# Kernel optimization log

Measured on AMD Instinct MI355X. Metric: run time of the kernel, lower is better.

## Reference

```python
import jax, jax.numpy as jnp
import numpy as np

NBITS = 16  # posit word size passed to posit_forward
ES = 1      # posit exponent-field size (standard posit16 uses es=1)


def posit_quant(x, nbits=NBITS, es=ES):
    """Round-trip float -> posit(nbits, es) -> float, vectorized.

    Emulates posit quantization: regime length determines how many fraction
    bits remain, mantissa is rounded to that precision, magnitude clamped to
    [minpos, maxpos]. Straight-through estimator keeps gradients useful.
    """
    absx = jnp.abs(x)
    sign = jnp.sign(x)
    safe = jnp.maximum(absx, 1e-30)
    scale = jnp.floor(jnp.log2(safe))                 # binary exponent
    useed_log2 = float(2 ** es)
    regime = jnp.floor(scale / useed_log2)
    rlen = jnp.where(regime >= 0, regime + 2.0, 1.0 - regime)  # regime bits
    fbits = jnp.clip(nbits - 1 - es - rlen, 0.0, 28.0)          # fraction bits left
    pw = jnp.exp2(fbits)
    m = safe * jnp.exp2(-scale)                       # mantissa in [1, 2)
    mq = 1.0 + jnp.round((m - 1.0) * pw) / pw
    maxscale = float((nbits - 2) * (2 ** es))         # maxpos = 2^((n-2)*2^es)
    mag = jnp.clip(mq * jnp.exp2(scale), jnp.exp2(-maxscale), jnp.exp2(maxscale))
    q = jnp.where(absx == 0.0, 0.0, sign * mag)
    return x + jax.lax.stop_gradient(q - x)           # straight-through


def posit_linear(x, W, b):
    # posit_forward: quantize operands, GEMM, quantize the accumulated output
    xq = posit_quant(x)
    Wq = posit_quant(W)
    bq = posit_quant(b)
    return posit_quant(xq @ Wq.T + bq)


def setup_inputs() -> dict:
    key = jax.random.key(0)
    ks = jax.random.split(key, 7)

    def w(k, o, i):
        return jax.random.normal(k, (o, i), jnp.float32) * (1.0 / np.sqrt(i))

    return {
        "x": jax.random.normal(ks[0], (4096, 2048), jnp.float32),
        "W0": w(ks[1], 8192, 2048),
        "b0": jax.random.normal(ks[2], (8192,), jnp.float32) * 0.01,
        "W1": w(ks[3], 8192, 8192),
        "b1": jax.random.normal(ks[4], (8192,), jnp.float32) * 0.01,
        "W2": w(ks[5], 2048, 8192),
        "b2": jax.random.normal(ks[6], (2048,), jnp.float32) * 0.01,
    }


def reference(x, W0, b0, W1, b1, W2, b2):
    # layer 0: posit linear + relu (clamp(min=0))
    h = jax.nn.relu(posit_linear(x, W0, b0))
    # layer 1: posit linear + relu
    h = jax.nn.relu(posit_linear(h, W1, b1))
    # layer 2: posit linear, identity activation
    return posit_linear(h, W2, b2)
```

## Files before the change

### kernel.cpp

```cpp
#include <hip/hip_runtime.h>
#include <hip/hip_bf16.h>
#include <cstdint>
#include <cstddef>

using bf16 = __hip_bfloat16;
typedef __attribute__((ext_vector_type(8))) short short8;
typedef __attribute__((ext_vector_type(4))) float f32x4;

__device__ __forceinline__ float posit_quant_f32(float x) {
  float absx = fabsf(x);
  float safe = fmaxf(absx, 1e-30f);
  uint32_t bits = __float_as_uint(safe);
  int scale = (int)((bits >> 23) & 0xFFu) - 127;
  int regime = scale >> 1;
  int rlen = (regime >= 0) ? (regime + 2) : (1 - regime);
  int fbits = 14 - rlen;
  fbits = fbits < 0 ? 0 : fbits;
  float pw = (float)(1 << fbits);
  float m = __uint_as_float((bits & 0x007FFFFFu) | 0x3F800000u);
  float mq = rintf((m - 1.0f) * pw) * (1.0f / pw) + 1.0f;
  float mag = mq * __uint_as_float((uint32_t)(scale + 127) << 23);
  mag = fminf(fmaxf(mag, 0x1p-28f), 0x1p28f);
  return (absx == 0.0f) ? 0.0f : copysignf(mag, x);
}

__device__ __forceinline__ ushort4 pq_bf16x4(float4 v) {
  ushort4 o;
  o.x = __builtin_bit_cast(unsigned short, __float2bfloat16(posit_quant_f32(v.x)));
  o.y = __builtin_bit_cast(unsigned short, __float2bfloat16(posit_quant_f32(v.y)));
  o.z = __builtin_bit_cast(unsigned short, __float2bfloat16(posit_quant_f32(v.z)));
  o.w = __builtin_bit_cast(unsigned short, __float2bfloat16(posit_quant_f32(v.w)));
  return o;
}

__global__ void kquant_all(const float* __restrict__ s0, bf16* __restrict__ d0,
                           const float* __restrict__ s1, bf16* __restrict__ d1,
                           const float* __restrict__ s2, bf16* __restrict__ d2,
                           const float* __restrict__ s3, bf16* __restrict__ d3,
                           long c0, long c1, long c2, long c3) {
  long i = (long)blockIdx.x * blockDim.x + threadIdx.x;
  long stride = (long)gridDim.x * blockDim.x;
  for (; i < c3; i += stride) {
    const float* s; bf16* d; long j;
    if (i < c0)      { s = s0; d = d0; j = i; }
    else if (i < c1) { s = s1; d = d1; j = i - c0; }
    else if (i < c2) { s = s2; d = d2; j = i - c1; }
    else             { s = s3; d = d3; j = i - c2; }
    float4 v = ((const float4*)s)[j];
    ((ushort4*)d)[j] = pq_bf16x4(v);
  }
}

__global__ void kcombine(const float* __restrict__ p, const float* __restrict__ bias,
                         float* __restrict__ out, long n4, long halfn, int cmask) {
  long i = (long)blockIdx.x * blockDim.x + threadIdx.x;
  long stride = (long)gridDim.x * blockDim.x;
  for (; i < n4; i += stride) {
    float4 a = ((const float4*)p)[i];
    float4 b = ((const float4*)(p + halfn))[i];
    int c0 = (int)(i & cmask) * 4;
    float4 o;
    o.x = posit_quant_f32(a.x + b.x + posit_quant_f32(bias[c0 + 0]));
    o.y = posit_quant_f32(a.y + b.y + posit_quant_f32(bias[c0 + 1]));
    o.z = posit_quant_f32(a.z + b.z + posit_quant_f32(bias[c0 + 2]));
    o.w = posit_quant_f32(a.w + b.w + posit_quant_f32(bias[c0 + 3]));
    ((float4*)out)[i] = o;
  }
}

typedef __attribute__((address_space(1))) uint32_t gu32;
typedef __attribute__((address_space(3))) uint32_t lu32;

#define SBAR()  do { __builtin_amdgcn_sched_barrier(0); __builtin_amdgcn_s_barrier(); \
                     __builtin_amdgcn_sched_barrier(0); } while (0)
#define VMCNT(N) asm volatile("s_waitcnt vmcnt(" #N ")" ::: "memory")

#define AB0 0
#define AB1 32768
#define BB0 65536
#define BB1 98304

#define STG(SRC, KT, H, DST) do { \
    const char* _s = (SRC) + (long)((H) * 128) * Kb + (long)(KT) * 128; \
    char* _d = smem + (DST) + (H) * 16384 + wave * 1024; \
    __builtin_amdgcn_global_load_lds((const gu32*)_s, (lu32*)_d, 16, 0, 0); \
    __builtin_amdgcn_global_load_lds((const gu32*)(_s + 64 * Kb), (lu32*)(_d + 8192), 16, 0, 0); \
  } while (0)

#define LDA8(AOFF, FI, CK) (*(const short8*)(smem + (AOFF) + aRel + (FI) * 2048 + (CK)))
#define LDB8(BOFF, FJ, CK) (*(const short8*)(smem + (BOFF) + bRel + (FJ) * 2048 + (CK)))

#define PREF_ALO(BUF) do { _Pragma("unroll") \
    for (int f = 0; f < 4; ++f) { ar[f][0] = LDA8(BUF, f, ck0); ar[f][1] = LDA8(BUF, f, ck1); } \
  } while (0)
#define PREF_AHI(BUF) do { _Pragma("unroll") \
    for (int f = 0; f < 4; ++f) { ar[f][0] = LDA8(BUF, f + 4, ck0); ar[f][1] = LDA8(BUF, f + 4, ck1); } \
  } while (0)
#define PREF_B01(BUF) do { _Pragma("unroll") \
    for (int f = 0; f < 2; ++f) { b01[f][0] = LDB8(BUF, f, ck0); b01[f][1] = LDB8(BUF, f, ck1); } \
  } while (0)
#define PREF_B23(BUF) do { _Pragma("unroll") \
    for (int f = 0; f < 2; ++f) { b23[f][0] = LDB8(BUF, f + 2, ck0); b23[f][1] = LDB8(BUF, f + 2, ck1); } \
  } while (0)

#define MQS(ACC0, BS, FJ0) do { \
    _Pragma("unroll") \
    for (int fi = 0; fi < 4; ++fi) { \
      _Pragma("unroll") \
      for (int fj = 0; fj < 2; ++fj) { \
        acc[(ACC0) + fi][(FJ0) + fj] = __builtin_amdgcn_mfma_f32_16x16x32_bf16( \
            ar[fi][0], BS[fj][0], acc[(ACC0) + fi][(FJ0) + fj], 0, 0, 0); \
        acc[(ACC0) + fi][(FJ0) + fj] = __builtin_amdgcn_mfma_f32_16x16x32_bf16( \
            ar[fi][1], BS[fj][1], acc[(ACC0) + fi][(FJ0) + fj], 0, 0, 0); \
      } \
    } \
  } while (0)

template <int MODE>
__global__ __launch_bounds__(512, 2) void gemm256_posit(
    const bf16* __restrict__ A, const bf16* __restrict__ B,
    const float* __restrict__ bias, void* __restrict__ out,
    int M, int N, int Kfull, int Kloop, int nbt, int cpx) {
  __shared__ __align__(1024) char smem[131072];

  const int tid  = threadIdx.x;
  const int lane = tid & 63;
  const int wave = tid >> 6;
  const int wr = wave >> 2;
  const int wc = wave & 3;

  const int flat = blockIdx.x;
  const int wgid = (flat & 7) * cpx + (flat >> 3);
  const int split = wgid / nbt;
  const int t = wgid - split * nbt;
  const int nbx = N >> 8;
  const long brow0 = (long)(t / nbx) * 256;
  const long bcol0 = (long)(t % nbx) * 256;

  const long Kb = (long)Kfull * 2;
  const long splitoff = (long)split * Kloop * 2;

  const int srow = tid >> 3;
  const int scb  = ((tid & 7) * 16) ^ (((tid >> 3) & 7) << 4);
  const char* srcA = (const char*)A + (brow0 + srow) * Kb + scb + splitoff;
  const char* srcB = (const char*)B + (bcol0 + srow) * Kb + scb + splitoff;

  const int fr  = lane & 15;
  const int swz = (lane & 7) << 4;
  const int ck0 = (((lane >> 4) << 4)) ^ swz;
  const int ck1 = (64 + ((lane >> 4) << 4)) ^ swz;
  const int aRel = wr * 16384 + fr * 128;
  const int bRel = wc * 8192 + fr * 128;

  f32x4 acc[8][4] = {};
  short8 ar[4][2], b01[2][2], b23[2][2];

  const int nkt = Kloop >> 6;
  const int np  = nkt >> 1;

  STG(srcB, 0, 0, BB0); STG(srcB, 0, 1, BB0);
  STG(srcA, 0, 0, AB0); STG(srcA, 0, 1, AB0);
  STG(srcB, 1, 0, BB1); STG(srcB, 1, 1, BB1);
  VMCNT(4);
  SBAR();
  PREF_ALO(AB0); PREF_B01(BB0);
  __builtin_amdgcn_sched_barrier(0);

#pragma unroll 1
  for (int i = 0; i < np; ++i) {
    const int kA1 = 2 * i + 1;
    const int kS2 = (2 * i + 2) & (nkt - 1);
    const int kS3 = (2 * i + 3) & (nkt - 1);

    PREF_B23(BB0);
    STG(srcA, kA1, 0, AB1);
    SBAR();
    __builtin_amdgcn_s_setprio(1); MQS(0, b01, 0); __builtin_amdgcn_s_setprio(0);
    SBAR();

    STG(srcA, kA1, 1, AB1);
    SBAR();
    __builtin_amdgcn_s_setprio(1); MQS(0, b23, 2); __builtin_amdgcn_s_setprio(0);
    PREF_AHI(AB0);
    SBAR();

    STG(srcB, kS2, 0, BB0);
    SBAR();
    __builtin_amdgcn_s_setprio(1); MQS(4, b01, 0); __builtin_amdgcn_s_setprio(0);
    SBAR();

    STG(srcB, kS2, 1, BB0);
    VMCNT(4);
    SBAR();
    __builtin_amdgcn_s_setprio(1); MQS(4, b23, 2); __builtin_amdgcn_s_setprio(0);
    PREF_ALO(AB1); PREF_B01(BB1);
    SBAR();

    PREF_B23(BB1);
    STG(srcA, kS2, 0, AB0);
    SBAR();
    __builtin_amdgcn_s_setprio(1); MQS(0, b01, 0); __builtin_amdgcn_s_setprio(0);
    SBAR();

    STG(srcA, kS2, 1, AB0);
    SBAR();
    __builtin_amdgcn_s_setprio(1); MQS(0, b23, 2); __builtin_amdgcn_s_setprio(0);
    PREF_AHI(AB1);
    SBAR();

    STG(srcB, kS3, 0, BB1);
    SBAR();
    __builtin_amdgcn_s_setprio(1); MQS(4, b01, 0); __builtin_amdgcn_s_setprio(0);
    SBAR();

    STG(srcB, kS3, 1, BB1);
    VMCNT(4);
    SBAR();
    __builtin_amdgcn_s_setprio(1); MQS(4, b23, 2); __builtin_amdgcn_s_setprio(0);
    PREF_ALO(AB0); PREF_B01(BB0);
    SBAR();
  }
  asm volatile("s_waitcnt vmcnt(0) lgkmcnt(0)" ::: "memory");

  const int orow = (lane >> 4) * 4;
  const long row0 = brow0 + wr * 128;
  const long col0 = bcol0 + wc * 64;
  const long obase = (MODE == 2) ? (long)split * M * N : 0;
#pragma unroll
  for (int fj = 0; fj < 4; ++fj) {
    const long col = col0 + fj * 16 + fr;
    const float bv = (MODE == 2) ? 0.0f : posit_quant_f32(bias[col]);
#pragma unroll
    for (int fi = 0; fi < 8; ++fi) {
#pragma unroll
      for (int q = 0; q < 4; ++q) {
        float v = acc[fi][fj][q];
        if (MODE != 2) {
          v = posit_quant_f32(v + bv);
          if (MODE == 0) v = fmaxf(v, 0.0f);
        }
        const long idx = obase + (row0 + fi * 16 + orow + q) * (long)N + col;
        if (MODE == 0) ((bf16*)out)[idx] = __float2bfloat16(v);
        else           ((float*)out)[idx] = v;
      }
    }
  }
}

#define GBM 128
#define GBN 128
#define GBK 32

__device__ __forceinline__ void gload_lds16(const void* g, void* l) {
  __builtin_amdgcn_global_load_lds((const gu32*)g, (lu32*)l, 16, 0, 0);
}

template <bool RELU, bool OUTBF16>
__global__ __launch_bounds__(256, 2) void gemm_bt_posit(
    const bf16* __restrict__ A, const bf16* __restrict__ B,
    const float* __restrict__ bias, void* __restrict__ out,
    int M, int N, int K) {
  __shared__ __align__(1024) bf16 sA[GBM][GBK];
  __shared__ __align__(1024) bf16 sB[GBN][GBK];

  const int tid = threadIdx.x;
  const int lane = tid & 63;
  const int wave = tid >> 6;
  const int wr = wave >> 1;
  const int wc = wave & 1;
  const long brow0 = (long)blockIdx.y * GBM;
  const long bcol0 = (long)blockIdx.x * GBN;

  const int srow = lane >> 2;
  const int scol = (lane & 3) * 8;
  const int seg0 = wave * 2;

  const bf16* gA0 = A + (brow0 + seg0 * 16 + srow) * (long)K + scol;
  const bf16* gA1 = A + (brow0 + seg0 * 16 + 16 + srow) * (long)K + scol;
  const bf16* gB0 = B + (bcol0 + seg0 * 16 + srow) * (long)K + scol;
  const bf16* gB1 = B + (bcol0 + seg0 * 16 + 16 + srow) * (long)K + scol;
  bf16* lA0 = (bf16*)sA + seg0 * 512;
  bf16* lA1 = lA0 + 512;
  bf16* lB0 = (bf16*)sB + seg0 * 512;
  bf16* lB1 = lB0 + 512;

  f32x4 acc[4][4] = {};
  const int fr = lane & 15;
  const int fk = (lane >> 4) * 8;

  for (int kt = 0; kt < K; kt += GBK) {
    __syncthreads();
    gload_lds16(gA0 + kt, lA0);
    gload_lds16(gA1 + kt, lA1);
    gload_lds16(gB0 + kt, lB0);
    gload_lds16(gB1 + kt, lB1);
    __syncthreads();

    short8 af[4], bfv[4];
#pragma unroll
    for (int i = 0; i < 4; ++i) af[i] = *(const short8*)&sA[wr * 64 + i * 16 + fr][fk];
#pragma unroll
    for (int j = 0; j < 4; ++j) bfv[j] = *(const short8*)&sB[wc * 64 + j * 16 + fr][fk];
#pragma unroll
    for (int i = 0; i < 4; ++i)
#pragma unroll
      for (int j = 0; j < 4; ++j)
        acc[i][j] = __builtin_amdgcn_mfma_f32_16x16x32_bf16(af[i], bfv[j], acc[i][j], 0, 0, 0);
  }

  const int orow = (lane >> 4) * 4;
  const long row0 = brow0 + wr * 64;
  const long col0 = bcol0 + wc * 64;
#pragma unroll
  for (int j = 0; j < 4; ++j) {
    const long col = col0 + j * 16 + fr;
    const float bv = posit_quant_f32(bias[col]);
#pragma unroll
    for (int i = 0; i < 4; ++i) {
#pragma unroll
      for (int q = 0; q < 4; ++q) {
        float v = posit_quant_f32(acc[i][j][q] + bv);
        if (RELU) v = fmaxf(v, 0.0f);
        const long idx = (row0 + i * 16 + orow + q) * (long)N + col;
        if (OUTBF16) ((bf16*)out)[idx] = __float2bfloat16(v);
        else         ((float*)out)[idx] = v;
      }
    }
  }
}

extern "C" void kernel_launch(void* const* d_in, const int* in_sizes, int n_in,
                              void* d_out, int out_size, void* d_ws, size_t ws_size,
                              hipStream_t stream) {
  const float* x  = (const float*)d_in[0];
  const float* W0 = (const float*)d_in[1];
  const float* b0 = (const float*)d_in[2];
  const float* W1 = (const float*)d_in[3];
  const float* b1 = (const float*)d_in[4];
  const float* W2 = (const float*)d_in[5];
  const float* b2 = (const float*)d_in[6];

  const int M = 4096, D0 = 2048, D1 = 8192, D2 = 8192, DO = 2048;

  char* ws = (char*)d_ws;
  size_t off = 0;
  auto alloc = [&](size_t bytes) {
    char* p = ws + off;
    off += (bytes + 255) & ~(size_t)255;
    return p;
  };
  bf16* xq  = (bf16*)alloc((size_t)M * D0 * 2);
  bf16* W0q = (bf16*)alloc((size_t)D1 * D0 * 2);
  bf16* W1q = (bf16*)alloc((size_t)D2 * D1 * 2);
  bf16* W2q = (bf16*)alloc((size_t)DO * D2 * 2);
  bf16* h0  = (bf16*)alloc((size_t)M * D1 * 2);
  bf16* h1  = (bf16*)alloc((size_t)M * D2 * 2);
  float* part = (float*)alloc((size_t)2 * M * DO * 4);
  const bool splitk = (off <= ws_size);
  (void)in_sizes; (void)n_in; (void)out_size;

  {
    long q0 = (long)M * D0 / 4;
    long q1 = q0 + (long)D1 * D0 / 4;
    long q2 = q1 + (long)D2 * D1 / 4;
    long q3 = q2 + (long)DO * D2 / 4;
    kquant_all<<<2048, 256, 0, stream>>>(x, xq, W0, W0q, W1, W1q, W2, W2q,
                                         q0, q1, q2, q3);
  }

  {
    int nbt = (D1 / 256) * (M / 256), nwg = nbt;
    gemm256_posit<0><<<dim3(nwg), dim3(512), 0, stream>>>(
        xq, W0q, b0, h0, M, D1, D0, D0, nbt, nwg / 8);
  }
  {
    int nbt = (D2 / 256) * (M / 256), nwg = nbt;
    gemm256_posit<0><<<dim3(nwg), dim3(512), 0, stream>>>(
        h0, W1q, b1, h1, M, D2, D1, D1, nbt, nwg / 8);
  }
  if (splitk) {
    int nbt = (DO / 256) * (M / 256);
    int nwg = nbt * 2;
    gemm256_posit<2><<<dim3(nwg), dim3(512), 0, stream>>>(
        h1, W2q, nullptr, part, M, DO, D2, D2 / 2, nbt, nwg / 8);
    long n4 = (long)M * DO / 4;
    kcombine<<<2048, 256, 0, stream>>>(part, b2, (float*)d_out, n4,
                                       (long)M * DO, DO / 4 - 1);
  } else {
    gemm_bt_posit<false, false><<<dim3(DO / GBN, M / GBM), dim3(256), 0, stream>>>(
        h1, W2q, b2, (float*)d_out, M, DO, D2);
  }
}
```

Measured before the change: 874.8 us.

## Simplify GEMM main loop to two-phase double buffering with full-tile MFMA bursts

Replaces the eight-phase interleaved schedule with a simpler two-phase double-buffered loop. Each phase waits for all outstanding global loads, does one barrier, issues the next tile's A and B loads, and runs full 4x4 MFMA bursts using a single B register set. The aim is to cut the many per-step barriers and their sync overhead. In exchange, each vmcnt(0) drains every global load, so copy latency is hidden less well than with the partial vmcnt(4) waits it replaces.

```diff
diff --git a/kernel.cpp b/kernel.cpp
--- a/kernel.cpp
+++ b/kernel.cpp
@@ -96,22 +96,19 @@
 #define PREF_AHI(BUF) do { _Pragma("unroll") \
     for (int f = 0; f < 4; ++f) { ar[f][0] = LDA8(BUF, f + 4, ck0); ar[f][1] = LDA8(BUF, f + 4, ck1); } \
   } while (0)
-#define PREF_B01(BUF) do { _Pragma("unroll") \
-    for (int f = 0; f < 2; ++f) { b01[f][0] = LDB8(BUF, f, ck0); b01[f][1] = LDB8(BUF, f, ck1); } \
-  } while (0)
-#define PREF_B23(BUF) do { _Pragma("unroll") \
-    for (int f = 0; f < 2; ++f) { b23[f][0] = LDB8(BUF, f + 2, ck0); b23[f][1] = LDB8(BUF, f + 2, ck1); } \
-  } while (0)
-
-#define MQS(ACC0, BS, FJ0) do { \
+#define PREF_B(BUF) do { _Pragma("unroll") \
+    for (int f = 0; f < 4; ++f) { br[f][0] = LDB8(BUF, f, ck0); br[f][1] = LDB8(BUF, f, ck1); } \
+  } while (0)
+
+#define MQALL(ACC0) do { \
     _Pragma("unroll") \
     for (int fi = 0; fi < 4; ++fi) { \
       _Pragma("unroll") \
-      for (int fj = 0; fj < 2; ++fj) { \
-        acc[(ACC0) + fi][(FJ0) + fj] = __builtin_amdgcn_mfma_f32_16x16x32_bf16( \
-            ar[fi][0], BS[fj][0], acc[(ACC0) + fi][(FJ0) + fj], 0, 0, 0); \
-        acc[(ACC0) + fi][(FJ0) + fj] = __builtin_amdgcn_mfma_f32_16x16x32_bf16( \
-            ar[fi][1], BS[fj][1], acc[(ACC0) + fi][(FJ0) + fj], 0, 0, 0); \
+      for (int fj = 0; fj < 4; ++fj) { \
+        acc[(ACC0) + fi][fj] = __builtin_amdgcn_mfma_f32_16x16x32_bf16( \
+            ar[fi][0], br[fj][0], acc[(ACC0) + fi][fj], 0, 0, 0); \
+        acc[(ACC0) + fi][fj] = __builtin_amdgcn_mfma_f32_16x16x32_bf16( \
+            ar[fi][1], br[fj][1], acc[(ACC0) + fi][fj], 0, 0, 0); \
       } \
     } \
   } while (0)
@@ -153,72 +150,36 @@
   const int bRel = wc * 8192 + fr * 128;
 
   f32x4 acc[8][4] = {};
-  short8 ar[4][2], b01[2][2], b23[2][2];
+  short8 ar[4][2], br[4][2];
 
   const int nkt = Kloop >> 6;
   const int np  = nkt >> 1;
 
+  STG(srcA, 0, 0, AB0); STG(srcA, 0, 1, AB0);
   STG(srcB, 0, 0, BB0); STG(srcB, 0, 1, BB0);
-  STG(srcA, 0, 0, AB0); STG(srcA, 0, 1, AB0);
-  STG(srcB, 1, 0, BB1); STG(srcB, 1, 1, BB1);
-  VMCNT(4);
-  SBAR();
-  PREF_ALO(AB0); PREF_B01(BB0);
-  __builtin_amdgcn_sched_barrier(0);
 
 #pragma unroll 1
   for (int i = 0; i < np; ++i) {
-    const int kA1 = 2 * i + 1;
-    const int kS2 = (2 * i + 2) & (nkt - 1);
-    const int kS3 = (2 * i + 3) & (nkt - 1);
-
-    PREF_B23(BB0);
-    STG(srcA, kA1, 0, AB1);
+    const int t1 = (2 * i + 1) & (nkt - 1);
+    const int t2 = (2 * i + 2) & (nkt - 1);
+
+    VMCNT(0);
     SBAR();
-    __builtin_amdgcn_s_setprio(1); MQS(0, b01, 0); __builtin_amdgcn_s_setprio(0);
+    STG(srcA, t1, 0, AB1); STG(srcA, t1, 1, AB1);
+    PREF_B(BB0); PREF_ALO(AB0);
+    __builtin_amdgcn_s_setprio(1); MQALL(0); __builtin_amdgcn_s_setprio(0);
+    STG(srcB, t1, 0, BB1); STG(srcB, t1, 1, BB1);
+    PREF_AHI(AB0);
+    __builtin_amdgcn_s_setprio(1); MQALL(4); __builtin_amdgcn_s_setprio(0);
+
+    VMCNT(0);
     SBAR();
-
-    STG(srcA, kA1, 1, AB1);
-    SBAR();
-    __builtin_amdgcn_s_setprio(1); MQS(0, b23, 2); __builtin_amdgcn_s_setprio(0);
-    PREF_AHI(AB0);
-    SBAR();
-
-    STG(srcB, kS2, 0, BB0);
-    SBAR();
-    __builtin_amdgcn_s_setprio(1); MQS(4, b01, 0); __builtin_amdgcn_s_setprio(0);
-    SBAR();
-
-    STG(srcB, kS2, 1, BB0);
-    VMCNT(4);
-    SBAR();
-    __builtin_amdgcn_s_setprio(1); MQS(4, b23, 2); __builtin_amdgcn_s_setprio(0);
-    PREF_ALO(AB1); PREF_B01(BB1);
-    SBAR();
-
-    PREF_B23(BB1);
-    STG(srcA, kS2, 0, AB0);
-    SBAR();
-    __builtin_amdgcn_s_setprio(1); MQS(0, b01, 0); __builtin_amdgcn_s_setprio(0);
-    SBAR();
-
-    STG(srcA, kS2, 1, AB0);
-    SBAR();
-    __builtin_amdgcn_s_setprio(1); MQS(0, b23, 2); __builtin_amdgcn_s_setprio(0);
+    STG(srcA, t2, 0, AB0); STG(srcA, t2, 1, AB0);
+    PREF_B(BB1); PREF_ALO(AB1);
+    __builtin_amdgcn_s_setprio(1); MQALL(0); __builtin_amdgcn_s_setprio(0);
+    STG(srcB, t2, 0, BB0); STG(srcB, t2, 1, BB0);
     PREF_AHI(AB1);
-    SBAR();
-
-    STG(srcB, kS3, 0, BB1);
-    SBAR();
-    __builtin_amdgcn_s_setprio(1); MQS(4, b01, 0); __builtin_amdgcn_s_setprio(0);
-    SBAR();
-
-    STG(srcB, kS3, 1, BB1);
-    VMCNT(4);
-    SBAR();
-    __builtin_amdgcn_s_setprio(1); MQS(4, b23, 2); __builtin_amdgcn_s_setprio(0);
-    PREF_ALO(AB0); PREF_B01(BB0);
-    SBAR();
+    __builtin_amdgcn_s_setprio(1); MQALL(4); __builtin_amdgcn_s_setprio(0);
   }
   asm volatile("s_waitcnt vmcnt(0) lgkmcnt(0)" ::: "memory");
 
```

Result: slower. 892.9 us (+2.1%).
